# Kernel optimization log

Hardware: AMD Instinct MI355X
Metric: run time of the kernel (lower is better)

The kernel has to match this reference:

```python
import jax, jax.numpy as jnp
import numpy as np

B, C, L = 32, 64, 2048
FREQ = L // 2 + 1            # 1025
BAND_SIZES = [341, 341, 343]  # freq//3, freq//3, remainder


def setup_inputs() -> dict:
    key = jax.random.key(0)
    k = jax.random.split(key, 6)
    X = jax.random.normal(k[0], (B, C, L), dtype=jnp.float32)
    A0 = jax.random.normal(k[1], (BAND_SIZES[0], BAND_SIZES[0]), dtype=jnp.float32)
    A1 = jax.random.normal(k[2], (BAND_SIZES[1], BAND_SIZES[1]), dtype=jnp.float32)
    A2 = jax.random.normal(k[3], (BAND_SIZES[2], BAND_SIZES[2]), dtype=jnp.float32)
    fusion_weights = jnp.ones((3,), dtype=jnp.float32)
    # Gumbel(0,1) noise for the 2-way gumbel-softmax over each (b, i, j) entry
    gumbel_noise = jax.random.gumbel(k[4], (B, C, C, 2), dtype=jnp.float32)
    return {"X": X, "A0": A0, "A1": A1, "A2": A2,
            "fusion_weights": fusion_weights, "gumbel_noise": gumbel_noise}


def _band_dist(band, A):
    # band: (b, c, s), A: (s, s). dist[b,i,j] = ||A (band_i - band_j)||^2
    # Gram trick: ||y_i - y_j||^2 = q_i + q_j - 2 y_i . y_j, y = band @ A^T
    Y = jnp.einsum('ds,bcs->bcd', A, band)          # (b, c, s)
    G = jnp.einsum('bid,bjd->bij', Y, Y)            # (b, c, c)
    q = jnp.einsum('bid,bid->bi', Y, Y)             # (b, c)
    dist = q[:, :, None] + q[:, None, :] - 2.0 * G
    return jnp.maximum(dist, 0.0)                   # guard fp round-off


def reference(X, A0, A1, A2, fusion_weights, gumbel_noise):
    XF = jnp.abs(jnp.fft.rfft(X, axis=-1))          # (b, c, FREQ)
    s0, s1, s2 = BAND_SIZES
    bands = (XF[..., :s0], XF[..., s0:s0 + s1], XF[..., s0 + s1:])
    As = (A0, A1, A2)
    dists = jnp.stack([_band_dist(b_, A_) for b_, A_ in zip(bands, As)], axis=-1)  # (b,c,c,3)
    w = jax.nn.softmax(fusion_weights)
    dist = jnp.einsum('bijk,k->bij', dists, w)      # (b, c, c)

    exp_dist = 1.0 / (dist + 1e-10)
    eye = jnp.eye(C, dtype=exp_dist.dtype)
    mask = 1.0 - eye
    exp_dist = exp_dist * mask
    exp_max = jax.lax.stop_gradient(jnp.max(exp_dist, axis=-1, keepdims=True))
    p = exp_dist / exp_max
    p = (p * mask + eye) * 0.99                     # probs in (0, 0.99]

    # Bernoulli via 2-class gumbel-softmax (hard, tau=1, straight-through)
    logits = jnp.stack([jnp.log(p / (1.0 - p)), jnp.log((1.0 - p) / p)], axis=-1)  # (b,c,c,2)
    y = logits + gumbel_noise
    y_soft = jax.nn.softmax(y, axis=-1)
    y_hard = jax.nn.one_hot(jnp.argmax(y, axis=-1), 2, dtype=y_soft.dtype)
    sample = (y_hard - jax.lax.stop_gradient(y_soft) + y_soft)[..., 0]  # (b,c,c)
    return sample[:, None, :, :]                    # (b, 1, c, c)
```

## Files before the change

### kernel.cpp

```cpp
#include <hip/hip_runtime.h>
#include <math.h>

#define Bn 32
#define Cn 64
#define Ln 2048
#define NFREQ 1025
#define S0c 341
#define S1c 341
#define S2c 343
#define KPAD 352
#define XROW (3 * 1056)
#define APLANE (3 * KPAD * KPAD)

#define PI_D 3.14159265358979323846

typedef unsigned short u16;
typedef __attribute__((ext_vector_type(4))) u16 u16x4;
typedef __attribute__((ext_vector_type(8))) short short8;
typedef __attribute__((ext_vector_type(4))) float f32x4;

#define PADIX(i) ((i) + ((i) >> 4))

__device__ __forceinline__ u16 rneb(float f) {
    unsigned u = __float_as_uint(f);
    unsigned r = (u + 0x7FFFu + ((u >> 16) & 1u)) >> 16;
    return (u16)r;
}
__device__ __forceinline__ float b2f(u16 h) {
    return __uint_as_float(((unsigned)h) << 16);
}
__device__ __forceinline__ void split3(float v, u16& h1, u16& h2, u16& h3) {
    h1 = rneb(v);
    float r1 = v - b2f(h1);
    h2 = rneb(r1);
    float r2 = r1 - b2f(h2);
    h3 = rneb(r2);
}

__device__ __forceinline__ int rev4_10(unsigned x) {
    unsigned t = __brev(x) >> 22;
    return (int)(((t & 0x155u) << 1) | ((t >> 1) & 0x155u));
}

__global__ __launch_bounds__(256) void k_prep(const float* __restrict__ A0,
                                              const float* __restrict__ A1,
                                              const float* __restrict__ A2,
                                              float2* __restrict__ tw,
                                              u16* __restrict__ AS) {
    int b = blockIdx.x;
    int tid = threadIdx.x;
    if (b < 8) {
        int t = b * 256 + tid;
        double ang = -2.0 * PI_D * (double)t / 2048.0;
        double s, c;
        sincos(ang, &s, &c);
        tw[t] = make_float2((float)c, (float)s);
        return;
    }
    int i = b - 8;
    int z = i / 484;
    const float* A = (z == 0) ? A0 : ((z == 1) ? A1 : A2);
    int S = (z == 2) ? S2c : S0c;
    int idx = (i % 484) * 256 + tid;
    int d = idx / KPAD, kk = idx - d * KPAD;
    float v = (d < S && kk < S) ? A[(size_t)d * S + kk] : 0.0f;
    u16 h1, h2, h3;
    split3(v, h1, h2, h3);
    size_t o = ((size_t)z * KPAD + d) * KPAD + kk;
    AS[o] = h1;
    AS[APLANE + o] = h2;
    AS[2 * (size_t)APLANE + o] = h3;
}

__global__ __launch_bounds__(256) void k_fft(const float* __restrict__ X,
                                             const float2* __restrict__ tw,
                                             u16* __restrict__ XS) {
    __shared__ float re[1088];
    __shared__ float im[1088];
    int row = blockIdx.x;
    int tid = threadIdx.x;
    {
        int k = tid;
        float2 w1 = tw[2 * k];
        float2 w2 = tw[4 * k];
        float2 w3 = tw[6 * k];
        int i0 = PADIX(k), i1 = PADIX(k + 256), i2 = PADIX(k + 512), i3 = PADIX(k + 768);
        const float2* xr = (const float2*)(X + (size_t)row * Ln);
        float2 v0 = xr[k];
        float2 v1 = xr[k + 256];
        float2 v2 = xr[k + 512];
        float2 v3 = xr[k + 768];
        float ar = v0.x, ai = v0.y;
        float br = v1.x, bi = v1.y;
        float cr = v2.x, ci = v2.y;
        float dr = v3.x, di = v3.y;
        float t0r = ar + cr, t0i = ai + ci;
        float t1r = ar - cr, t1i = ai - ci;
        float t2r = br + dr, t2i = bi + di;
        float t3r = br - dr, t3i = bi - di;
        re[i0] = t0r + t2r; im[i0] = t0i + t2i;
        float u1r = t1r + t3i, u1i = t1i - t3r;
        re[i1] = u1r * w1.x - u1i * w1.y; im[i1] = u1r * w1.y + u1i * w1.x;
        float u2r = t0r - t2r, u2i = t0i - t2i;
        re[i2] = u2r * w2.x - u2i * w2.y; im[i2] = u2r * w2.y + u2i * w2.x;
        float u3r = t1r - t3i, u3i = t1i + t3r;
        re[i3] = u3r * w3.x - u3i * w3.y; im[i3] = u3r * w3.y + u3i * w3.x;
    }
    __syncthreads();
    #pragma unroll
    for (int s = 1; s < 5; ++s) {
        int log2Q = 8 - 2 * s;
        int Q = 1 << log2Q;
        int k = tid & (Q - 1);
        int g = tid >> log2Q;
        int base = (g << (log2Q + 2)) + k;
        int i0 = PADIX(base), i1 = PADIX(base + Q), i2 = PADIX(base + 2 * Q), i3 = PADIX(base + 3 * Q);
        int step = 2 << (2 * s);
        float2 w1 = tw[k * step];
        float2 w2 = tw[2 * k * step];
        float2 w3 = tw[3 * k * step];
        float ar = re[i0], ai = im[i0];
        float br = re[i1], bi = im[i1];
        float cr = re[i2], ci = im[i2];
        float dr = re[i3], di = im[i3];
        float t0r = ar + cr, t0i = ai + ci;
        float t1r = ar - cr, t1i = ai - ci;
        float t2r = br + dr, t2i = bi + di;
        float t3r = br - dr, t3i = bi - di;
        re[i0] = t0r + t2r; im[i0] = t0i + t2i;
        float u1r = t1r + t3i, u1i = t1i - t3r;
        re[i1] = u1r * w1.x - u1i * w1.y; im[i1] = u1r * w1.y + u1i * w1.x;
        float u2r = t0r - t2r, u2i = t0i - t2i;
        re[i2] = u2r * w2.x - u2i * w2.y; im[i2] = u2r * w2.y + u2i * w2.x;
        float u3r = t1r - t3i, u3i = t1i + t3r;
        re[i3] = u3r * w3.x - u3i * w3.y; im[i3] = u3r * w3.y + u3i * w3.x;
        __syncthreads();
    }
    u16* xrow = XS + (size_t)row * XROW;
    if (tid < 31) {
        int pp = (tid < 11) ? (341 + tid) : ((tid < 22) ? (682 + tid) : (1025 + tid));
        xrow[pp] = 0; xrow[1056 + pp] = 0; xrow[2112 + pp] = 0;
    }
    for (int k = tid; k <= 1024; k += 256) {
        float Xr, Xi;
        if (k == 0)        { Xr = re[0] + im[0]; Xi = 0.0f; }
        else if (k == 1024){ Xr = re[0] - im[0]; Xi = 0.0f; }
        else {
            int rv  = PADIX(rev4_10((unsigned)k));
            int rv2 = PADIX(rev4_10((unsigned)(1024 - k)));
            float2 t = tw[k];
            float Zr = re[rv],  Zi = im[rv];
            float Wr = re[rv2], Wi = im[rv2];
            float Er = 0.5f * (Zr + Wr), Ei = 0.5f * (Zi - Wi);
            float Or = 0.5f * (Zi + Wi), Oi = -0.5f * (Zr - Wr);
            Xr = Er + t.x * Or - t.y * Oi;
            Xi = Ei + t.x * Oi + t.y * Or;
        }
        float v = sqrtf(Xr * Xr + Xi * Xi);
        int zb = (k < S0c) ? 0 : ((k < S0c + S1c) ? 1 : 2);
        int pos = k + 11 * zb;
        u16 h1, h2, h3;
        split3(v, h1, h2, h3);
        xrow[pos] = h1;
        xrow[1056 + pos] = h2;
        xrow[2112 + pos] = h3;
    }
}

__global__ __launch_bounds__(256) void k_gemm(const u16* __restrict__ XS,
                                              const u16* __restrict__ AS,
                                              float* __restrict__ Y) {
    const int Sarr[3] = {S0c, S1c, S2c};
    const int Oarr[3] = {0, S0c, S0c + S1c};
    int z = blockIdx.z;
    int S = Sarr[z], O = Oarr[z];

    __shared__ u16 sX1[64][40], sX2[64][40], sX3[64][40];
    __shared__ u16 sA1[32][40], sA2[32][40], sA3[32][40];

    int r0 = blockIdx.x * 64;
    int d0 = blockIdx.y * 32;
    int tid = threadIdx.x;
    int lane = tid & 63, w = tid >> 6;
    int wm = (w >> 1) * 32, wn = (w & 1) * 16;
    int fm = lane & 15, kq = lane >> 4;
    int row8 = tid >> 3, seg4 = (tid & 7) * 4;

    f32x4 z4 = {0.0f, 0.0f, 0.0f, 0.0f};
    short8 aone, afm;
    {
        u16 hone = 0x3F80;
        u16 hfm = rneb((float)fm);
        #pragma unroll
        for (int j = 0; j < 8; ++j) { aone[j] = (short)hone; afm[j] = (short)hfm; }
    }
    f32x4 calR = __builtin_amdgcn_mfma_f32_16x16x32_bf16(afm, aone, z4, 0, 0, 0);
    f32x4 calC = __builtin_amdgcn_mfma_f32_16x16x32_bf16(aone, afm, z4, 0, 0, 0);
    int rIdx[4], cIdx[4];
    #pragma unroll
    for (int i = 0; i < 4; ++i) {
        rIdx[i] = (int)(calR[i] * 0.03125f + 0.5f);
        cIdx[i] = (int)(calC[i] * 0.03125f + 0.5f);
    }

    const u16* xb0 = XS + (size_t)(r0 + row8) * XROW + (size_t)z * KPAD + seg4;
    const u16* xb1 = xb0 + 32 * (size_t)XROW;
    const u16* ab  = AS + ((size_t)z * KPAD + (d0 + row8)) * KPAD + seg4;

    u16x4 wxa1, wxa2, wxa3, wxb1, wxb2, wxb3, wa1, wa2, wa3;
    auto load_tile = [&](int st) {
        int ko = st * 32;
        wxa1 = *(const u16x4*)(xb0 + ko);
        wxa2 = *(const u16x4*)(xb0 + 1056 + ko);
        wxa3 = *(const u16x4*)(xb0 + 2112 + ko);
        wxb1 = *(const u16x4*)(xb1 + ko);
        wxb2 = *(const u16x4*)(xb1 + 1056 + ko);
        wxb3 = *(const u16x4*)(xb1 + 2112 + ko);
        wa1  = *(const u16x4*)(ab + ko);
        wa2  = *(const u16x4*)(ab + APLANE + ko);
        wa3  = *(const u16x4*)(ab + 2 * (size_t)APLANE + ko);
    };

    double acc0[4] = {0.0, 0.0, 0.0, 0.0};
    double acc1[4] = {0.0, 0.0, 0.0, 0.0};
    load_tile(0);
    const int nsteps = KPAD / 32;
    for (int st = 0; st < nsteps; ++st) {
        __syncthreads();
        *(u16x4*)&sX1[row8][seg4] = wxa1;
        *(u16x4*)&sX2[row8][seg4] = wxa2;
        *(u16x4*)&sX3[row8][seg4] = wxa3;
        *(u16x4*)&sX1[row8 + 32][seg4] = wxb1;
        *(u16x4*)&sX2[row8 + 32][seg4] = wxb2;
        *(u16x4*)&sX3[row8 + 32][seg4] = wxb3;
        *(u16x4*)&sA1[row8][seg4] = wa1;
        *(u16x4*)&sA2[row8][seg4] = wa2;
        *(u16x4*)&sA3[row8][seg4] = wa3;
        __syncthreads();
        if (st + 1 < nsteps) load_tile(st + 1);
        short8 b1 = *(const short8*)&sA1[wn + fm][kq * 8];
        short8 b2 = *(const short8*)&sA2[wn + fm][kq * 8];
        short8 b3 = *(const short8*)&sA3[wn + fm][kq * 8];
        {
            short8 a1 = *(const short8*)&sX1[wm + fm][kq * 8];
            short8 a2 = *(const short8*)&sX2[wm + fm][kq * 8];
            short8 a3 = *(const short8*)&sX3[wm + fm][kq * 8];
            f32x4 p1 = __builtin_amdgcn_mfma_f32_16x16x32_bf16(a1, b1, z4, 0, 0, 0);
            f32x4 p2 = __builtin_amdgcn_mfma_f32_16x16x32_bf16(a1, b2, z4, 0, 0, 0);
            p2 = __builtin_amdgcn_mfma_f32_16x16x32_bf16(a2, b1, p2, 0, 0, 0);
            p2 = __builtin_amdgcn_mfma_f32_16x16x32_bf16(a1, b3, p2, 0, 0, 0);
            p2 = __builtin_amdgcn_mfma_f32_16x16x32_bf16(a2, b2, p2, 0, 0, 0);
            p2 = __builtin_amdgcn_mfma_f32_16x16x32_bf16(a3, b1, p2, 0, 0, 0);
            #pragma unroll
            for (int i = 0; i < 4; ++i) acc0[i] += (double)p1[i] + (double)p2[i];
        }
        {
            short8 a1 = *(const short8*)&sX1[wm + 16 + fm][kq * 8];
            short8 a2 = *(const short8*)&sX2[wm + 16 + fm][kq * 8];
            short8 a3 = *(const short8*)&sX3[wm + 16 + fm][kq * 8];
            f32x4 p1 = __builtin_amdgcn_mfma_f32_16x16x32_bf16(a1, b1, z4, 0, 0, 0);
            f32x4 p2 = __builtin_amdgcn_mfma_f32_16x16x32_bf16(a1, b2, z4, 0, 0, 0);
            p2 = __builtin_amdgcn_mfma_f32_16x16x32_bf16(a2, b1, p2, 0, 0, 0);
            p2 = __builtin_amdgcn_mfma_f32_16x16x32_bf16(a1, b3, p2, 0, 0, 0);
            p2 = __builtin_amdgcn_mfma_f32_16x16x32_bf16(a2, b2, p2, 0, 0, 0);
            p2 = __builtin_amdgcn_mfma_f32_16x16x32_bf16(a3, b1, p2, 0, 0, 0);
            #pragma unroll
            for (int i = 0; i < 4; ++i) acc1[i] += (double)p1[i] + (double)p2[i];
        }
    }
    #pragma unroll
    for (int i = 0; i < 4; ++i) {
        int d = d0 + wn + cIdx[i];
        if (d < S) {
            Y[(size_t)(r0 + wm + rIdx[i]) * NFREQ + O + d] = (float)acc0[i];
            Y[(size_t)(r0 + wm + 16 + rIdx[i]) * NFREQ + O + d] = (float)acc1[i];
        }
    }
}

__global__ __launch_bounds__(256) void k_distdecide(const float* __restrict__ Y,
                                                    const float* __restrict__ fw,
                                                    const float* __restrict__ gum,
                                                    float* __restrict__ out) {
    __shared__ u16 sY1[64][40], sY2[64][40], sY3[64][40];
    __shared__ double sG[16][66];
    __shared__ double qp[64][8];
    __shared__ double qv[64];

    int b = blockIdx.x;
    int s = blockIdx.y;
    int tid = threadIdx.x;
    int lane = tid & 63, w = tid >> 6;
    int fm = lane & 15, kq = lane >> 4;
    int r = tid >> 3, seg = (tid & 7) * 4;

    double f0 = (double)fw[0], f1 = (double)fw[1], f2 = (double)fw[2];
    double m = fmax(f0, fmax(f1, f2));
    double e0 = exp(f0 - m), e1 = exp(f1 - m), e2 = exp(f2 - m);
    double esum = e0 + e1 + e2;
    float sw0f = (float)sqrt(e0 / esum), sw1f = (float)sqrt(e1 / esum), sw2f = (float)sqrt(e2 / esum);

    f32x4 z4 = {0.0f, 0.0f, 0.0f, 0.0f};
    short8 aone, afm;
    {
        u16 hone = 0x3F80;
        u16 hfm = rneb((float)fm);
        #pragma unroll
        for (int j = 0; j < 8; ++j) { aone[j] = (short)hone; afm[j] = (short)hfm; }
    }
    f32x4 calR = __builtin_amdgcn_mfma_f32_16x16x32_bf16(afm, aone, z4, 0, 0, 0);
    f32x4 calC = __builtin_amdgcn_mfma_f32_16x16x32_bf16(aone, afm, z4, 0, 0, 0);
    int rIdx[4], cIdx[4];
    #pragma unroll
    for (int i = 0; i < 4; ++i) {
        rIdx[i] = (int)(calR[i] * 0.03125f + 0.5f);
        cIdx[i] = (int)(calC[i] * 0.03125f + 0.5f);
    }

    const float* Yb = Y + (size_t)b * Cn * NFREQ;
    double qa = 0.0, qb = 0.0;
    u16x4 wa1, wa2, wa3, wb1, wb2, wb3;
    auto load_tile = [&](int st) {
        int k0 = st * 32 + seg;
        #pragma unroll
        for (int j = 0; j < 4; ++j) {
            int d = k0 + j;
            bool dv = d < NFREQ;
            float sw = dv ? ((d < S0c) ? sw0f : ((d < S0c + S1c) ? sw1f : sw2f)) : 0.0f;
            float va = dv ? Yb[(size_t)r * NFREQ + d] * sw : 0.0f;
            float vb = dv ? Yb[(size_t)(r + 32) * NFREQ + d] * sw : 0.0f;
            qa += (double)va * (double)va;
            qb += (double)vb * (double)vb;
            u16 h1, h2, h3;
            split3(va, h1, h2, h3); wa1[j] = h1; wa2[j] = h2; wa3[j] = h3;
            split3(vb, h1, h2, h3); wb1[j] = h1; wb2[j] = h2; wb3[j] = h3;
        }
    };

    double acc[4] = {0.0, 0.0, 0.0, 0.0};
    load_tile(0);
    const int nsteps = 33;
    for (int st = 0; st < nsteps; ++st) {
        __syncthreads();
        *(u16x4*)&sY1[r][seg] = wa1;
        *(u16x4*)&sY2[r][seg] = wa2;
        *(u16x4*)&sY3[r][seg] = wa3;
        *(u16x4*)&sY1[r + 32][seg] = wb1;
        *(u16x4*)&sY2[r + 32][seg] = wb2;
        *(u16x4*)&sY3[r + 32][seg] = wb3;
        __syncthreads();
        if (st + 1 < nsteps) load_tile(st + 1);
        short8 a1 = *(const short8*)&sY1[s * 16 + fm][kq * 8];
        short8 a2 = *(const short8*)&sY2[s * 16 + fm][kq * 8];
        short8 a3 = *(const short8*)&sY3[s * 16 + fm][kq * 8];
        short8 b1 = *(const short8*)&sY1[w * 16 + fm][kq * 8];
        short8 b2 = *(const short8*)&sY2[w * 16 + fm][kq * 8];
        short8 b3 = *(const short8*)&sY3[w * 16 + fm][kq * 8];
        f32x4 p1 = __builtin_amdgcn_mfma_f32_16x16x32_bf16(a1, b1, z4, 0, 0, 0);
        f32x4 p2 = __builtin_amdgcn_mfma_f32_16x16x32_bf16(a1, b2, z4, 0, 0, 0);
        p2 = __builtin_amdgcn_mfma_f32_16x16x32_bf16(a2, b1, p2, 0, 0, 0);
        p2 = __builtin_amdgcn_mfma_f32_16x16x32_bf16(a1, b3, p2, 0, 0, 0);
        p2 = __builtin_amdgcn_mfma_f32_16x16x32_bf16(a2, b2, p2, 0, 0, 0);
        p2 = __builtin_amdgcn_mfma_f32_16x16x32_bf16(a3, b1, p2, 0, 0, 0);
        #pragma unroll
        for (int i = 0; i < 4; ++i) acc[i] += (double)p1[i] + (double)p2[i];
    }
    #pragma unroll
    for (int i = 0; i < 4; ++i)
        sG[rIdx[i]][w * 16 + cIdx[i]] = acc[i];
    qp[r][tid & 7] = qa;
    qp[r + 32][tid & 7] = qb;
    __syncthreads();
    if (tid < 64) {
        double q = 0.0;
        #pragma unroll
        for (int c = 0; c < 8; ++c) q += qp[tid][c];
        qv[tid] = q;
    }
    __syncthreads();

    const float* gb = gum + (size_t)b * 8192;
    float* ob = out + (size_t)b * 4096;
    #pragma unroll
    for (int pass = 0; pass < 4; ++pass) {
        int il = pass * 4 + (tid >> 6);
        int i = s * 16 + il;
        int j = tid & 63;
        double g = sG[il][j];
        double dist = fmax(qv[i] + qv[j] - 2.0 * g, 0.0);
        double e = (i == j) ? 0.0 : 1.0 / (dist + 1e-10);
        double emax = e;
        #pragma unroll
        for (int off = 32; off; off >>= 1)
            emax = fmax(emax, __shfl_xor(emax, off, 64));
        double p = (i == j) ? 0.99 : (e / emax) * 0.99;
        double l0 = log(p / (1.0 - p));
        int idx = i * 64 + j;
        double y0 = l0 + (double)gb[2 * idx];
        double y1 = -l0 + (double)gb[2 * idx + 1];
        ob[idx] = (y0 >= y1) ? 1.0f : 0.0f;
    }
}

extern "C" void kernel_launch(void* const* d_in, const int* in_sizes, int n_in,
                              void* d_out, int out_size, void* d_ws, size_t ws_size,
                              hipStream_t stream) {
    const float* X  = (const float*)d_in[0];
    const float* A0 = (const float*)d_in[1];
    const float* A1 = (const float*)d_in[2];
    const float* A2 = (const float*)d_in[3];
    const float* fw = (const float*)d_in[4];
    const float* gm = (const float*)d_in[5];
    float* out = (float*)d_out;

    char* ws = (char*)d_ws;
    float2* tw = (float2*)(ws);
    u16*  XS = (u16*)(ws + 32768);
    u16*  AS = (u16*)(ws + 13008896);
    float* Y = (float*)(ws + 15239168);

    k_prep<<<1460, 256, 0, stream>>>(A0, A1, A2, tw, AS);
    k_fft<<<Bn * Cn, 256, 0, stream>>>(X, tw, XS);
    k_gemm<<<dim3(32, 11, 3), 256, 0, stream>>>(XS, AS, Y);
    k_distdecide<<<dim3(Bn, 4), 256, 0, stream>>>(Y, fw, gm, out);
}
```

Before: 140.0 us.

## Emit split-bf16 scaled Y from GEMM and compute full Gram per batch block

The GEMM epilogue now applies the softmax fusion-weight scaling and writes Y directly as three padded bf16 split planes. This removes the per-element scaling and splitting that the distance kernel used to do with fp32 loads. The distance kernel now uses one block per batch that computes the whole 64x64 Gram. It takes the squared norms from the Gram diagonal, which avoids recomputing the loads across four row-slab blocks but leaves only 32 blocks in that launch. The prep kernel gains extra blocks that zero the padding columns of the Y planes.

```diff
diff --git a/kernel.cpp b/kernel.cpp
--- a/kernel.cpp
+++ b/kernel.cpp
@@ -46,7 +46,8 @@
                                               const float* __restrict__ A1,
                                               const float* __restrict__ A2,
                                               float2* __restrict__ tw,
-                                              u16* __restrict__ AS) {
+                                              u16* __restrict__ AS,
+                                              u16* __restrict__ YS) {
     int b = blockIdx.x;
     int tid = threadIdx.x;
     if (b < 8) {
@@ -57,19 +58,29 @@
         tw[t] = make_float2((float)c, (float)s);
         return;
     }
-    int i = b - 8;
-    int z = i / 484;
-    const float* A = (z == 0) ? A0 : ((z == 1) ? A1 : A2);
-    int S = (z == 2) ? S2c : S0c;
-    int idx = (i % 484) * 256 + tid;
-    int d = idx / KPAD, kk = idx - d * KPAD;
-    float v = (d < S && kk < S) ? A[(size_t)d * S + kk] : 0.0f;
-    u16 h1, h2, h3;
-    split3(v, h1, h2, h3);
-    size_t o = ((size_t)z * KPAD + d) * KPAD + kk;
-    AS[o] = h1;
-    AS[APLANE + o] = h2;
-    AS[2 * (size_t)APLANE + o] = h3;
+    if (b < 1460) {
+        int i = b - 8;
+        int z = i / 484;
+        const float* A = (z == 0) ? A0 : ((z == 1) ? A1 : A2);
+        int S = (z == 2) ? S2c : S0c;
+        int idx = (i % 484) * 256 + tid;
+        int d = idx / KPAD, kk = idx - d * KPAD;
+        float v = (d < S && kk < S) ? A[(size_t)d * S + kk] : 0.0f;
+        u16 h1, h2, h3;
+        split3(v, h1, h2, h3);
+        size_t o = ((size_t)z * KPAD + d) * KPAD + kk;
+        AS[o] = h1;
+        AS[APLANE + o] = h2;
+        AS[2 * (size_t)APLANE + o] = h3;
+        return;
+    }
+    int idx = (b - 1460) * 256 + tid;
+    if (idx < 2048 * 93) {
+        int row = idx / 93, pr = idx - row * 93;
+        int plane = pr / 31, pi = pr - plane * 31;
+        int col = (pi < 11) ? (341 + pi) : ((pi < 22) ? (682 + pi) : (1025 + pi));
+        YS[(size_t)row * XROW + plane * 1056 + col] = 0;
+    }
 }
 
 __global__ __launch_bounds__(256) void k_fft(const float* __restrict__ X,
@@ -169,11 +180,11 @@
 
 __global__ __launch_bounds__(256) void k_gemm(const u16* __restrict__ XS,
                                               const u16* __restrict__ AS,
-                                              float* __restrict__ Y) {
+                                              const float* __restrict__ fw,
+                                              u16* __restrict__ YS) {
     const int Sarr[3] = {S0c, S1c, S2c};
-    const int Oarr[3] = {0, S0c, S0c + S1c};
     int z = blockIdx.z;
-    int S = Sarr[z], O = Oarr[z];
+    int S = Sarr[z];
 
     __shared__ u16 sX1[64][40], sX2[64][40], sX3[64][40];
     __shared__ u16 sA1[32][40], sA2[32][40], sA3[32][40];
@@ -185,6 +196,13 @@
     int wm = (w >> 1) * 32, wn = (w & 1) * 16;
     int fm = lane & 15, kq = lane >> 4;
     int row8 = tid >> 3, seg4 = (tid & 7) * 4;
+
+    double f0 = (double)fw[0], f1 = (double)fw[1], f2 = (double)fw[2];
+    double mfw = fmax(f0, fmax(f1, f2));
+    double e0 = exp(f0 - mfw), e1 = exp(f1 - mfw), e2 = exp(f2 - mfw);
+    double esum = e0 + e1 + e2;
+    float swf = (z == 0) ? (float)sqrt(e0 / esum)
+              : (z == 1) ? (float)sqrt(e1 / esum) : (float)sqrt(e2 / esum);
 
     f32x4 z4 = {0.0f, 0.0f, 0.0f, 0.0f};
     short8 aone, afm;
@@ -272,33 +290,31 @@
     for (int i = 0; i < 4; ++i) {
         int d = d0 + wn + cIdx[i];
         if (d < S) {
-            Y[(size_t)(r0 + wm + rIdx[i]) * NFREQ + O + d] = (float)acc0[i];
-            Y[(size_t)(r0 + wm + 16 + rIdx[i]) * NFREQ + O + d] = (float)acc1[i];
+            int ra = r0 + wm + rIdx[i];
+            float ya = (float)acc0[i] * swf;
+            float yb = (float)acc1[i] * swf;
+            u16 h1, h2, h3;
+            size_t oa = (size_t)ra * XROW + (size_t)z * KPAD + d;
+            split3(ya, h1, h2, h3);
+            YS[oa] = h1; YS[oa + 1056] = h2; YS[oa + 2112] = h3;
+            size_t ob = oa + 16 * (size_t)XROW;
+            split3(yb, h1, h2, h3);
+            YS[ob] = h1; YS[ob + 1056] = h2; YS[ob + 2112] = h3;
         }
     }
 }
 
-__global__ __launch_bounds__(256) void k_distdecide(const float* __restrict__ Y,
-                                                    const float* __restrict__ fw,
+__global__ __launch_bounds__(256) void k_distdecide(const u16* __restrict__ YS,
                                                     const float* __restrict__ gum,
                                                     float* __restrict__ out) {
     __shared__ u16 sY1[64][40], sY2[64][40], sY3[64][40];
-    __shared__ double sG[16][66];
-    __shared__ double qp[64][8];
+    __shared__ double sG[64][66];
     __shared__ double qv[64];
-
     int b = blockIdx.x;
-    int s = blockIdx.y;
     int tid = threadIdx.x;
     int lane = tid & 63, w = tid >> 6;
     int fm = lane & 15, kq = lane >> 4;
     int r = tid >> 3, seg = (tid & 7) * 4;
-
-    double f0 = (double)fw[0], f1 = (double)fw[1], f2 = (double)fw[2];
-    double m = fmax(f0, fmax(f1, f2));
-    double e0 = exp(f0 - m), e1 = exp(f1 - m), e2 = exp(f2 - m);
-    double esum = e0 + e1 + e2;
-    float sw0f = (float)sqrt(e0 / esum), sw1f = (float)sqrt(e1 / esum), sw2f = (float)sqrt(e2 / esum);
 
     f32x4 z4 = {0.0f, 0.0f, 0.0f, 0.0f};
     short8 aone, afm;
@@ -317,27 +333,20 @@
         cIdx[i] = (int)(calC[i] * 0.03125f + 0.5f);
     }
 
-    const float* Yb = Y + (size_t)b * Cn * NFREQ;
-    double qa = 0.0, qb = 0.0;
+    const u16* yb0 = YS + (size_t)(b * 64 + r) * XROW + seg;
+    const u16* yb1 = yb0 + 32 * (size_t)XROW;
     u16x4 wa1, wa2, wa3, wb1, wb2, wb3;
     auto load_tile = [&](int st) {
-        int k0 = st * 32 + seg;
-        #pragma unroll
-        for (int j = 0; j < 4; ++j) {
-            int d = k0 + j;
-            bool dv = d < NFREQ;
-            float sw = dv ? ((d < S0c) ? sw0f : ((d < S0c + S1c) ? sw1f : sw2f)) : 0.0f;
-            float va = dv ? Yb[(size_t)r * NFREQ + d] * sw : 0.0f;
-            float vb = dv ? Yb[(size_t)(r + 32) * NFREQ + d] * sw : 0.0f;
-            qa += (double)va * (double)va;
-            qb += (double)vb * (double)vb;
-            u16 h1, h2, h3;
-            split3(va, h1, h2, h3); wa1[j] = h1; wa2[j] = h2; wa3[j] = h3;
-            split3(vb, h1, h2, h3); wb1[j] = h1; wb2[j] = h2; wb3[j] = h3;
-        }
+        int ko = st * 32;
+        wa1 = *(const u16x4*)(yb0 + ko);
+        wa2 = *(const u16x4*)(yb0 + 1056 + ko);
+        wa3 = *(const u16x4*)(yb0 + 2112 + ko);
+        wb1 = *(const u16x4*)(yb1 + ko);
+        wb2 = *(const u16x4*)(yb1 + 1056 + ko);
+        wb3 = *(const u16x4*)(yb1 + 2112 + ko);
     };
 
-    double acc[4] = {0.0, 0.0, 0.0, 0.0};
+    double acc[4][4] = {{0.0,0.0,0.0,0.0},{0.0,0.0,0.0,0.0},{0.0,0.0,0.0,0.0},{0.0,0.0,0.0,0.0}};
     load_tile(0);
     const int nsteps = 33;
     for (int st = 0; st < nsteps; ++st) {
@@ -350,43 +359,40 @@
         *(u16x4*)&sY3[r + 32][seg] = wb3;
         __syncthreads();
         if (st + 1 < nsteps) load_tile(st + 1);
-        short8 a1 = *(const short8*)&sY1[s * 16 + fm][kq * 8];
-        short8 a2 = *(const short8*)&sY2[s * 16 + fm][kq * 8];
-        short8 a3 = *(const short8*)&sY3[s * 16 + fm][kq * 8];
         short8 b1 = *(const short8*)&sY1[w * 16 + fm][kq * 8];
         short8 b2 = *(const short8*)&sY2[w * 16 + fm][kq * 8];
         short8 b3 = *(const short8*)&sY3[w * 16 + fm][kq * 8];
-        f32x4 p1 = __builtin_amdgcn_mfma_f32_16x16x32_bf16(a1, b1, z4, 0, 0, 0);
-        f32x4 p2 = __builtin_amdgcn_mfma_f32_16x16x32_bf16(a1, b2, z4, 0, 0, 0);
-        p2 = __builtin_amdgcn_mfma_f32_16x16x32_bf16(a2, b1, p2, 0, 0, 0);
-        p2 = __builtin_amdgcn_mfma_f32_16x16x32_bf16(a1, b3, p2, 0, 0, 0);
-        p2 = __builtin_amdgcn_mfma_f32_16x16x32_bf16(a2, b2, p2, 0, 0, 0);
-        p2 = __builtin_amdgcn_mfma_f32_16x16x32_bf16(a3, b1, p2, 0, 0, 0);
         #pragma unroll
-        for (int i = 0; i < 4; ++i) acc[i] += (double)p1[i] + (double)p2[i];
-    }
-    #pragma unroll
-    for (int i = 0; i < 4; ++i)
-        sG[rIdx[i]][w * 16 + cIdx[i]] = acc[i];
-    qp[r][tid & 7] = qa;
-    qp[r + 32][tid & 7] = qb;
+        for (int t = 0; t < 4; ++t) {
+            short8 a1 = *(const short8*)&sY1[t * 16 + fm][kq * 8];
+            short8 a2 = *(const short8*)&sY2[t * 16 + fm][kq * 8];
+            short8 a3 = *(const short8*)&sY3[t * 16 + fm][kq * 8];
+            f32x4 p1 = __builtin_amdgcn_mfma_f32_16x16x32_bf16(a1, b1, z4, 0, 0, 0);
+            f32x4 p2 = __builtin_amdgcn_mfma_f32_16x16x32_bf16(a1, b2, z4, 0, 0, 0);
+            p2 = __builtin_amdgcn_mfma_f32_16x16x32_bf16(a2, b1, p2, 0, 0, 0);
+            p2 = __builtin_amdgcn_mfma_f32_16x16x32_bf16(a1, b3, p2, 0, 0, 0);
+            p2 = __builtin_amdgcn_mfma_f32_16x16x32_bf16(a2, b2, p2, 0, 0, 0);
+            p2 = __builtin_amdgcn_mfma_f32_16x16x32_bf16(a3, b1, p2, 0, 0, 0);
+            #pragma unroll
+            for (int i = 0; i < 4; ++i) acc[t][i] += (double)p1[i] + (double)p2[i];
+        }
+    }
+    #pragma unroll
+    for (int t = 0; t < 4; ++t)
+        #pragma unroll
+        for (int i = 0; i < 4; ++i)
+            sG[t * 16 + rIdx[i]][w * 16 + cIdx[i]] = acc[t][i];
     __syncthreads();
-    if (tid < 64) {
-        double q = 0.0;
-        #pragma unroll
-        for (int c = 0; c < 8; ++c) q += qp[tid][c];
-        qv[tid] = q;
-    }
+    if (tid < 64) qv[tid] = sG[tid][tid];
     __syncthreads();
 
     const float* gb = gum + (size_t)b * 8192;
     float* ob = out + (size_t)b * 4096;
     #pragma unroll
-    for (int pass = 0; pass < 4; ++pass) {
-        int il = pass * 4 + (tid >> 6);
-        int i = s * 16 + il;
+    for (int pass = 0; pass < 16; ++pass) {
+        int i = pass * 4 + (tid >> 6);
         int j = tid & 63;
-        double g = sG[il][j];
+        double g = sG[i][j];
         double dist = fmax(qv[i] + qv[j] - 2.0 * g, 0.0);
         double e = (i == j) ? 0.0 : 1.0 / (dist + 1e-10);
         double emax = e;
@@ -417,10 +423,10 @@
     float2* tw = (float2*)(ws);
     u16*  XS = (u16*)(ws + 32768);
     u16*  AS = (u16*)(ws + 13008896);
-    float* Y = (float*)(ws + 15239168);
-
-    k_prep<<<1460, 256, 0, stream>>>(A0, A1, A2, tw, AS);
+    u16*  YS = (u16*)(ws + 15239168);
+
+    k_prep<<<2204, 256, 0, stream>>>(A0, A1, A2, tw, AS, YS);
     k_fft<<<Bn * Cn, 256, 0, stream>>>(X, tw, XS);
-    k_gemm<<<dim3(32, 11, 3), 256, 0, stream>>>(XS, AS, Y);
-    k_distdecide<<<dim3(Bn, 4), 256, 0, stream>>>(Y, fw, gm, out);
-}
+    k_gemm<<<dim3(32, 11, 3), 256, 0, stream>>>(XS, AS, fw, YS);
+    k_distdecide<<<Bn, 256, 0, stream>>>(YS, gm, out);
+}
```

After: 147.7 us. +5.5%, slower.
